# Optimization experiments

Hardware: AMD Instinct MI355X
Metric: run time of the kernel (lower is better)

The kernel has to match this reference:

```python
import jax, jax.numpy as jnp
import numpy as np

B, N, C, H, NL, NH = 8, 1024, 256, 512, 3, 8


def setup_inputs() -> dict:
    key = jax.random.key(0)
    ks = jax.random.split(key, 16)
    g = lambda k, shape: jax.random.normal(k, shape, jnp.float32) * 0.02
    return dict(
        concept_features=jax.random.normal(ks[0], (B, N, C), jnp.float32),
        adjacency_matrix=jax.random.uniform(ks[1], (B, N, N), jnp.float32),
        edge_types=jax.random.randint(ks[2], (B, N, N), 0, 10),
        concept_mask=jnp.ones((B, N), bool),
        W_emb=g(ks[3], (H, C)), b_emb=jnp.zeros((H,), jnp.float32),
        W_in=g(ks[4], (NL, 3 * H, H)), b_in=jnp.zeros((NL, 3 * H), jnp.float32),
        W_out=g(ks[5], (NL, H, H)), b_out=jnp.zeros((NL, H), jnp.float32),
        W_conv=g(ks[6], (NL, H, H)), b_conv=jnp.zeros((NL, H), jnp.float32),
        W_cls=g(ks[7], (1, H)), b_cls=jnp.zeros((1,), jnp.float32),
        W_diff=g(ks[8], (5, H)), b_diff=jnp.zeros((5,), jnp.float32),
        W_pre=g(ks[9], (1, 2 * H)), b_pre=jnp.zeros((1,), jnp.float32),
        W_pool=g(ks[10], (H, H)), b_pool=jnp.zeros((H,), jnp.float32),
    )


def reference(concept_features, adjacency_matrix, edge_types, concept_mask,
              W_emb, b_emb, W_in, b_in, W_out, b_out, W_conv, b_conv,
              W_cls, b_cls, W_diff, b_diff, W_pre, b_pre, W_pool, b_pool):
    Bq, Nc, _ = concept_features.shape
    Hd = W_emb.shape[0]
    dh = Hd // NH

    def mha(x, Wi, bi, Wo, bo):
        # torch nn.MultiheadAttention with batch_first=False: the (B,N,H)
        # input is treated as (seq=B, batch=N, embed=H) -> attention over B.
        qkv = x @ Wi.T + bi                      # (B,N,3H)
        q, k, v = jnp.split(qkv, 3, axis=-1)
        rs = lambda t: t.reshape(Bq, Nc, NH, dh)
        q, k, v = rs(q), rs(k), rs(v)
        sc = jnp.einsum('inhd,jnhd->nhij', q, k) / jnp.sqrt(jnp.float32(dh))
        a = jax.nn.softmax(sc, axis=-1)          # (N,NH,B,B)
        o = jnp.einsum('nhij,jnhd->inhd', a, v).reshape(Bq, Nc, Hd)
        return o @ Wo.T + bo

    def ln(x):  # F.layer_norm, no affine
        m = x.mean(-1, keepdims=True)
        v = ((x - m) ** 2).mean(-1, keepdims=True)
        return (x - m) * jax.lax.rsqrt(v + 1e-5)

    x = concept_features @ W_emb.T + b_emb       # (B,N,H)
    for l in range(W_in.shape[0]):
        att = mha(x, W_in[l], b_in[l], W_out[l], b_out[l])
        conv = att @ W_conv[l].T + b_conv[l]
        agg = jnp.einsum('bij,bjh->bih', adjacency_matrix, conv)
        x = ln(x + agg)

    mastery = x @ W_cls.T + b_cls                # (B,N,1)
    diff = x @ W_diff.T + b_diff                 # (B,N,5)

    # O(N^2) pairwise loop -> bilinear decomposition:
    # score(i,j) = x_i @ W_pre[:, :H].T + x_j @ W_pre[:, H:].T + b
    h1 = (x @ W_pre[:, :Hd].T)[..., 0]           # (B,N)
    h2 = (x @ W_pre[:, Hd:].T)[..., 0]           # (B,N)
    pair = h1[:, :, None] + h2[:, None, :] + b_pre[0]  # (B,N,N)
    off = ~np.eye(Nc, dtype=bool).reshape(-1)    # static mask, i!=j row-major
    prereq = pair.reshape(Bq, Nc * Nc)[:, off][..., None]  # (B,N*(N-1),1)

    graph = x.mean(axis=1) @ W_pool.T + b_pool   # (B,H)
    return (x, mastery, diff, prereq, graph)
```

## Files before the change

kernel.cpp:

```cpp
#include <hip/hip_runtime.h>
#include <hip/hip_bf16.h>

typedef unsigned short ushort_t;
typedef __attribute__((ext_vector_type(4))) float floatx4;
typedef __attribute__((ext_vector_type(8))) __bf16 bf16x8;
typedef __attribute__((ext_vector_type(4))) unsigned short ushortx4;
typedef __attribute__((ext_vector_type(8))) unsigned short ushortx8;

static __device__ __forceinline__ float b2f(ushort_t u) {
  union { unsigned int i; float f; } v; v.i = ((unsigned int)u) << 16; return v.f;
}
static __device__ __forceinline__ ushort_t f2b(float f) {
  unsigned int x = __float_as_uint(f);
  unsigned int r = (x + 0x7fffu + ((x >> 16) & 1u)) >> 16;
  return (ushort_t)r;
}
static __device__ __forceinline__ void glds16(const ushort_t* g, ushort_t* l) {
  __builtin_amdgcn_global_load_lds(
      (const __attribute__((address_space(1))) unsigned int*)g,
      (__attribute__((address_space(3))) unsigned int*)l, 16, 0, 0);
}

template<int MODE, bool ASPLIT, bool SPLITK>
__global__ __launch_bounds__(256, 3) void gemm_bt(
    const void* __restrict__ Ap, const ushort_t* __restrict__ Bm,
    const float* __restrict__ bias,
    float* __restrict__ CoutF, float* __restrict__ CoutF2,
    ushort_t* __restrict__ CoutB, ushort_t* __restrict__ CoutB2,
    int M, int N, int K, long aBatch, long bBatch, long cBatch)
{
  __shared__ __align__(16) ushort_t As[128 * 64];
  __shared__ __align__(16) ushort_t Bs[128 * 64];

  const int tid  = threadIdx.x;
  const int wid  = tid >> 6;
  const int lane = tid & 63;
  const int quad = lane >> 4;
  const int l16  = lane & 15;
  const int lin = blockIdx.y * gridDim.x + blockIdx.x;
  const int m0 = (lin % gridDim.y) * 128;
  const int n0 = (lin / gridDim.y) * 128;
  const int z  = SPLITK ? (blockIdx.z >> 1) : blockIdx.z;
  const int kh = SPLITK ? (blockIdx.z & 1) : 0;
  const int kbeg = SPLITK ? kh * (K >> 1) : 0;
  const int kend = SPLITK ? kbeg + (K >> 1) : K;
  float*    outF = (SPLITK && kh) ? CoutF2 : CoutF;
  ushort_t* outB = (SPLITK && kh) ? CoutB2 : CoutB;

  const ushort_t* Ab = (const ushort_t*)Ap + (long)z * aBatch;
  const float*    Af = (const float*)Ap + (long)z * aBatch;
  Bm += (long)z * bBatch;

  const int wr = (wid >> 1) * 64;
  const int wc = (wid & 1) * 64;

  const int srow = tid >> 3, ssub = (tid & 7) * 8;
  const long abase = (long)(m0 + srow) * K + ssub;
  const long bbase = (long)(n0 + srow) * K + ssub;

  floatx4 acc[4][4];
#pragma unroll
  for (int i = 0; i < 4; ++i)
#pragma unroll
    for (int j = 0; j < 4; ++j) acc[i][j] = (floatx4){0.f, 0.f, 0.f, 0.f};

  for (int k0 = kbeg; k0 < kend; k0 += 64) {
    __syncthreads();
    if constexpr (ASPLIT) {
#pragma unroll
      for (int p = 0; p < 4; ++p)
        glds16(Ab + abase + 32 * p * (long)K + k0, &As[tid * 8 + p * 2048]);
    } else {
#pragma unroll
      for (int p = 0; p < 8; ++p) {
        int c = tid + p * 256;
        int row = c >> 4, sub = (c & 15) * 4;
        floatx4 va = *(const floatx4*)(Af + (long)(m0 + row) * K + k0 + sub);
        ushortx4 ah;
#pragma unroll
        for (int r = 0; r < 4; ++r) ah[r] = f2b(va[r]);
        *(ushortx4*)(&As[row * 64 + sub]) = ah;
      }
    }
#pragma unroll
    for (int p = 0; p < 4; ++p)
      glds16(Bm + bbase + 32 * p * (long)K + k0, &Bs[tid * 8 + p * 2048]);
    __syncthreads();

#pragma unroll
    for (int kk = 0; kk < 2; ++kk) {
      bf16x8 a[4], b[4];
#pragma unroll
      for (int i = 0; i < 4; ++i)
        a[i] = *(const bf16x8*)(&As[(wr + i * 16 + l16) * 64 + kk * 32 + quad * 8]);
#pragma unroll
      for (int j = 0; j < 4; ++j)
        b[j] = *(const bf16x8*)(&Bs[(wc + j * 16 + l16) * 64 + kk * 32 + quad * 8]);
#pragma unroll
      for (int i = 0; i < 4; ++i)
#pragma unroll
        for (int j = 0; j < 4; ++j)
          acc[i][j] = __builtin_amdgcn_mfma_f32_16x16x32_bf16(a[i], b[j], acc[i][j], 0, 0, 0);
    }
  }

#pragma unroll
  for (int j = 0; j < 4; ++j) {
    int col = n0 + wc + j * 16 + l16;
    float bv = (bias != nullptr) ? bias[col] : 0.f;
#pragma unroll
    for (int i = 0; i < 4; ++i) {
      int mbase = m0 + wr + i * 16 + quad * 4;
      if constexpr (MODE == 0) {
#pragma unroll
        for (int r = 0; r < 4; ++r)
          outF[(long)z * cBatch + (long)(mbase + r) * N + col] = acc[i][j][r] + bv;
      } else if constexpr (MODE == 1) {
#pragma unroll
        for (int r = 0; r < 4; ++r)
          outB[(long)z * cBatch + (long)(mbase + r) * N + col] = f2b(acc[i][j][r] + bv);
      } else {
        int b = mbase >> 10, jrow = mbase & 1023;
        ushortx4 pk;
#pragma unroll
        for (int r = 0; r < 4; ++r) pk[r] = f2b(acc[i][j][r] + bv);
        *(ushortx4*)(CoutB + ((long)b * N + col) * 1024 + jrow) = pk;
      }
    }
  }
}

__global__ __launch_bounds__(256) void prep_kernel(
    const float* __restrict__ Win,  ushort_t* __restrict__ Winb,
    const float* __restrict__ Wemb, ushort_t* __restrict__ Wembb,
    const float* __restrict__ Wconv, ushort_t* __restrict__ Wcb,
    const float* __restrict__ ADJ,  ushort_t* __restrict__ ADJb,
    float* __restrict__ xm)
{
  const int bid = blockIdx.x, tid = threadIdx.x;
  const float* src; ushort_t* dst; long i;
  if (bid < 1152)      { src = Win;   dst = Winb;  i = (long)bid * 256 + tid; }
  else if (bid < 1216) { src = Wemb;  dst = Wembb; i = (long)(bid - 1152) * 256 + tid; }
  else if (bid < 1600) { src = Wconv; dst = Wcb;   i = (long)(bid - 1216) * 256 + tid; }
  else if (bid < 5696) { src = ADJ;   dst = ADJb;  i = (long)(bid - 1600) * 256 + tid; }
  else { xm[(bid - 5696) * 256 + tid] = 0.f; return; }
  floatx4 a = ((const floatx4*)src)[2 * i];
  floatx4 b = ((const floatx4*)src)[2 * i + 1];
  ushortx4 ha, hb;
#pragma unroll
  for (int r = 0; r < 4; ++r) { ha[r] = f2b(a[r]); hb[r] = f2b(b[r]); }
  ((ushortx4*)dst)[2 * i] = ha; ((ushortx4*)dst)[2 * i + 1] = hb;
}

__global__ __launch_bounds__(256) void transpose_split_kernel(
    const float* __restrict__ W, ushort_t* __restrict__ T)
{
  __shared__ float tile[64][65];
  const int k0 = blockIdx.x * 64, j0 = blockIdx.y * 64;
  const long base = (long)blockIdx.z * 262144;
  const int tid = threadIdx.x;
#pragma unroll
  for (int p = 0; p < 16; ++p) {
    int idx = tid + p * 256;
    int jj = idx >> 6, kk = idx & 63;
    tile[jj][kk] = W[base + (long)(j0 + jj) * 512 + k0 + kk];
  }
  __syncthreads();
#pragma unroll
  for (int p = 0; p < 16; ++p) {
    int idx = tid + p * 256;
    int kk = idx >> 6, jj = idx & 63;
    T[base + (long)(k0 + kk) * 512 + j0 + jj] = f2b(tile[jj][kk]);
  }
}

__global__ __launch_bounds__(256) void bfuse_kernel(
    const float* __restrict__ Wconv, const float* __restrict__ bout,
    const float* __restrict__ bconv, float* __restrict__ bf)
{
  const int w = threadIdx.x >> 6, lane = threadIdx.x & 63;
  const int gi = blockIdx.x * 4 + w;
  const int l = gi >> 9, o = gi & 511;
  float p = 0.f;
#pragma unroll
  for (int k = 0; k < 8; ++k)
    p += Wconv[(long)l * 262144 + (long)o * 512 + lane + 64 * k] *
         bout[l * 512 + lane + 64 * k];
#pragma unroll
  for (int msk = 1; msk <= 32; msk <<= 1) p += __shfl_xor(p, msk);
  if (lane == 0) bf[gi] = p + bconv[l * 512 + o];
}

__global__ __launch_bounds__(512) void attn_kernel(
    const ushort_t* __restrict__ qkv, ushort_t* __restrict__ outp)
{
  __shared__ float qs[8 * 1540];
  __shared__ float aw[8][64];
  const int tid = threadIdx.x;
  const int n = blockIdx.x;

  const ushort_t* src = qkv + (long)n * 1536;
#pragma unroll
  for (int p = 0; p < 3; ++p) {
    int c = tid + p * 512;
    int i = c / 192, off = (c % 192) * 8;
    ushortx8 u = *(const ushortx8*)(src + (long)i * 1024 * 1536 + off);
    float* d = &qs[i * 1540 + off];
#pragma unroll
    for (int r = 0; r < 8; ++r) d[r] = b2f(u[r]);
  }
  __syncthreads();

  const int h    = tid >> 6;
  const int lane = tid & 63;
  const int i = lane >> 3, j = lane & 7;
  float s = 0.f;
#pragma unroll 8
  for (int d = 0; d < 64; ++d)
    s += qs[i * 1540 + h * 64 + d] * qs[j * 1540 + 512 + h * 64 + d];
  s *= 0.125f;

  float m = s;
  m = fmaxf(m, __shfl_xor(m, 1));
  m = fmaxf(m, __shfl_xor(m, 2));
  m = fmaxf(m, __shfl_xor(m, 4));
  float e = __expf(s - m);
  float sum = e;
  sum += __shfl_xor(sum, 1);
  sum += __shfl_xor(sum, 2);
  sum += __shfl_xor(sum, 4);
  aw[h][lane] = e / sum;

  const long ob = (long)n * 512 + h * 64 + lane;
#pragma unroll
  for (int ii = 0; ii < 8; ++ii) {
    float acc = 0.f;
#pragma unroll
    for (int jj = 0; jj < 8; ++jj)
      acc += aw[h][ii * 8 + jj] * qs[jj * 1540 + 1024 + h * 64 + lane];
    outp[ob + (long)ii * 1024 * 512] = f2b(acc);
  }
}

__global__ __launch_bounds__(256) void ln_kernel(
    const ushort_t* __restrict__ xb,
    const ushort_t* __restrict__ aggA, const ushort_t* __restrict__ aggB,
    ushort_t* __restrict__ outB)
{
  const int w = threadIdx.x >> 6, lane = threadIdx.x & 63;
  const long base = ((long)blockIdx.x * 4 + w) * 512;
  float v[8];
  float s = 0.f;
#pragma unroll
  for (int k = 0; k < 8; ++k) {
    long idx = base + lane + 64 * k;
    v[k] = b2f(xb[idx]) + b2f(aggA[idx]) + b2f(aggB[idx]);
    s += v[k];
  }
#pragma unroll
  for (int msk = 1; msk <= 32; msk <<= 1) s += __shfl_xor(s, msk);
  float mean = s * (1.f / 512.f);
  float vv = 0.f;
#pragma unroll
  for (int k = 0; k < 8; ++k) { float d = v[k] - mean; vv += d * d; }
#pragma unroll
  for (int msk = 1; msk <= 32; msk <<= 1) vv += __shfl_xor(vv, msk);
  float inv = rsqrtf(vv * (1.f / 512.f) + 1e-5f);
#pragma unroll
  for (int k = 0; k < 8; ++k)
    outB[base + lane + 64 * k] = f2b((v[k] - mean) * inv);
}

__global__ __launch_bounds__(256) void final_ln_heads_kernel(
    const ushort_t* __restrict__ xb,
    const ushort_t* __restrict__ aggA, const ushort_t* __restrict__ aggB,
    float* __restrict__ out_x,
    const float* __restrict__ Wcls, const float* __restrict__ bcls,
    const float* __restrict__ Wdiff, const float* __restrict__ bdiff,
    const float* __restrict__ Wpre,
    float* __restrict__ mastery, float* __restrict__ diff,
    float* __restrict__ h1, float* __restrict__ h2)
{
  const int w = threadIdx.x >> 6, lane = threadIdx.x & 63;
  const long row = (long)blockIdx.x * 4 + w;
  const long base = row * 512;
  float v[8];
  float s = 0.f;
#pragma unroll
  for (int k = 0; k < 8; ++k) {
    long idx = base + lane + 64 * k;
    v[k] = b2f(xb[idx]) + b2f(aggA[idx]) + b2f(aggB[idx]);
    s += v[k];
  }
#pragma unroll
  for (int msk = 1; msk <= 32; msk <<= 1) s += __shfl_xor(s, msk);
  float mean = s * (1.f / 512.f);
  float vv = 0.f;
#pragma unroll
  for (int k = 0; k < 8; ++k) { float d = v[k] - mean; vv += d * d; }
#pragma unroll
  for (int msk = 1; msk <= 32; msk <<= 1) vv += __shfl_xor(vv, msk);
  float inv = rsqrtf(vv * (1.f / 512.f) + 1e-5f);
#pragma unroll
  for (int k = 0; k < 8; ++k) {
    v[k] = (v[k] - mean) * inv;
    out_x[base + lane + 64 * k] = v[k];
  }
#pragma unroll
  for (int o = 0; o < 8; ++o) {
    const float* wp = (o == 0) ? Wcls
                    : (o <= 5) ? (Wdiff + (o - 1) * 512)
                    : (o == 6) ? Wpre : (Wpre + 512);
    float p = 0.f;
#pragma unroll
    for (int k = 0; k < 8; ++k) p += v[k] * wp[lane + 64 * k];
#pragma unroll
    for (int msk = 1; msk <= 32; msk <<= 1) p += __shfl_xor(p, msk);
    if (lane == 0) {
      if (o == 0)      mastery[row] = p + bcls[0];
      else if (o <= 5) diff[row * 5 + (o - 1)] = p + bdiff[o - 1];
      else if (o == 6) h1[row] = p;
      else             h2[row] = p;
    }
  }
}

__global__ __launch_bounds__(256) void epi_kernel(
    const float* __restrict__ h1, const float* __restrict__ h2,
    const float* __restrict__ bpre, float* __restrict__ outp,
    const float* __restrict__ x, float* __restrict__ xm)
{
  const int bid = blockIdx.x;
  if (bid < 8192) {
    const int b = bid >> 10, i = bid & 1023;
    const float base = h1[b * 1024 + i] + bpre[0];
    const long ob = (long)b * (1024 * 1023) + (long)i * 1023;
#pragma unroll
    for (int r = 0; r < 4; ++r) {
      int j = r * 256 + threadIdx.x;
      if (j == i) continue;
      int pos = (j < i) ? j : j - 1;
      outp[ob + pos] = base + h2[b * 1024 + j];
    }
  } else {
    const int pb = bid - 8192;
    const int b = pb >> 5, cc = (pb >> 4) & 1, ns = pb & 15;
    const int c = cc * 256 + threadIdx.x;
    float s = 0.f;
    for (int n = ns * 64; n < ns * 64 + 64; ++n)
      s += x[((long)b * 1024 + n) * 512 + c];
    atomicAdd(&xm[b * 512 + c], s);
  }
}

__global__ __launch_bounds__(256) void graph_kernel(
    const float* __restrict__ xm, const float* __restrict__ Wpool,
    const float* __restrict__ bpool, float* __restrict__ g)
{
  const int gi = blockIdx.x * 256 + threadIdx.x;
  const int b = gi >> 9, o = gi & 511;
  float s = 0.f;
  for (int hh = 0; hh < 512; ++hh) s += xm[b * 512 + hh] * Wpool[o * 512 + hh];
  g[gi] = s * (1.f / 1024.f) + bpool[o];
}

extern "C" void kernel_launch(void* const* d_in, const int* in_sizes, int n_in,
                              void* d_out, int out_size, void* d_ws, size_t ws_size,
                              hipStream_t stream)
{
  const float* CF    = (const float*)d_in[0];
  const float* ADJ   = (const float*)d_in[1];
  const float* Wemb  = (const float*)d_in[4];
  const float* bemb  = (const float*)d_in[5];
  const float* Win   = (const float*)d_in[6];
  const float* bin   = (const float*)d_in[7];
  const float* Wout  = (const float*)d_in[8];
  const float* bout  = (const float*)d_in[9];
  const float* Wconv = (const float*)d_in[10];
  const float* bconv = (const float*)d_in[11];
  const float* Wcls  = (const float*)d_in[12];
  const float* bcls  = (const float*)d_in[13];
  const float* Wdiff = (const float*)d_in[14];
  const float* bdiff = (const float*)d_in[15];
  const float* Wpre  = (const float*)d_in[16];
  const float* bpre  = (const float*)d_in[17];
  const float* Wpool = (const float*)d_in[18];
  const float* bpool = (const float*)d_in[19];

  ushort_t* W = (ushort_t*)d_ws;
  ushort_t* xb   = W;
  ushort_t* qkvb = W + 4194304;
  ushort_t* cT    = qkvb;
  ushort_t* aggA  = qkvb + 4194304;
  ushort_t* aggB  = qkvb + 8388608;
  ushort_t* WoT   = qkvb + 4194304;
  ushort_t* Wembb = qkvb + 4980736;
  ushort_t* Wcb   = qkvb + 5111808;
  ushort_t* Winb = W + 16777216;
  ushort_t* Wfb  = W + 19136512;
  ushort_t* ADJb = W + 19922944;
  float* bfused = (float*)(W + 28311552);
  float* h1     = bfused + 1536;
  float* h2     = h1 + 8192;
  float* xm     = h2 + 8192;

  float* out_x       = (float*)d_out;
  float* out_mastery = out_x + 4194304;
  float* out_diff    = out_mastery + 8192;
  float* out_prereq  = out_diff + 40960;
  float* out_graph   = out_prereq + 8380416;
  ushort_t* aob = (ushort_t*)out_x;

  dim3 blk(256);

  prep_kernel<<<dim3(5712), blk, 0, stream>>>(Win, Winb, Wemb, Wembb,
                                              Wconv, Wcb, ADJ, ADJb, xm);
  transpose_split_kernel<<<dim3(8, 8, 3), blk, 0, stream>>>(Wout, WoT);
  gemm_bt<1, true, false><<<dim3(4, 4, 3), blk, 0, stream>>>(
      Wcb, WoT, nullptr, nullptr, nullptr, Wfb, nullptr,
      512, 512, 512, 262144, 262144, 262144);
  bfuse_kernel<<<dim3(384), blk, 0, stream>>>(Wconv, bout, bconv, bfused);

  gemm_bt<1, false, false><<<dim3(4, 64, 1), blk, 0, stream>>>(
      CF, Wembb, bemb, nullptr, nullptr, xb, nullptr, 8192, 512, 256, 0, 0, 0);

  for (int l = 0; l < 3; ++l) {
    gemm_bt<1, true, false><<<dim3(12, 64, 1), blk, 0, stream>>>(
        xb, Winb + (long)l * 786432, bin + l * 1536,
        nullptr, nullptr, qkvb, nullptr, 8192, 1536, 512, 0, 0, 0);
    attn_kernel<<<dim3(1024), dim3(512), 0, stream>>>(qkvb, aob);
    gemm_bt<2, true, false><<<dim3(4, 64, 1), blk, 0, stream>>>(
        aob, Wfb + (long)l * 262144, bfused + l * 512,
        nullptr, nullptr, cT, nullptr, 8192, 512, 512, 0, 0, 0);
    gemm_bt<1, true, true><<<dim3(4, 8, 16), blk, 0, stream>>>(
        ADJb, cT, nullptr, nullptr, nullptr, aggA, aggB,
        1024, 512, 1024, 1048576, 524288, 524288);
    if (l < 2)
      ln_kernel<<<dim3(2048), blk, 0, stream>>>(xb, aggA, aggB, xb);
    else
      final_ln_heads_kernel<<<dim3(2048), blk, 0, stream>>>(
          xb, aggA, aggB, out_x, Wcls, bcls, Wdiff, bdiff, Wpre,
          out_mastery, out_diff, h1, h2);
  }

  epi_kernel<<<dim3(8448), blk, 0, stream>>>(h1, h2, bpre, out_prereq,
                                             out_x, xm);
  graph_kernel<<<dim3(16), blk, 0, stream>>>(xm, Wpool, bpool, out_graph);
}
```

Before: 457.9 us.

## Swizzle GEMM LDS layout, split adjacency GEMM K four ways, fuse prep kernels

Applies an XOR swizzle to the LDS tile layout in the GEMM, used both for the global-to-LDS loads and the MFMA fragment reads, to avoid LDS bank conflicts. The adjacency aggregation GEMM goes from a 2-way to a 4-way split-K for more parallelism. The extra partial sums are staged in the prereq output buffer before it is written, and the layernorm kernels sum all four partials. The weight transpose and fused-bias kernels are folded into the prep kernel to save launches. The trade is more bf16 partial traffic and one more rounding step in the aggregation sum.

```diff
diff --git a/kernel.cpp b/kernel.cpp
--- a/kernel.cpp
+++ b/kernel.cpp
@@ -21,12 +21,12 @@
       (__attribute__((address_space(3))) unsigned int*)l, 16, 0, 0);
 }
 
-template<int MODE, bool ASPLIT, bool SPLITK>
+template<int MODE, bool ASPLIT, int KS>
 __global__ __launch_bounds__(256, 3) void gemm_bt(
     const void* __restrict__ Ap, const ushort_t* __restrict__ Bm,
     const float* __restrict__ bias,
-    float* __restrict__ CoutF, float* __restrict__ CoutF2,
-    ushort_t* __restrict__ CoutB, ushort_t* __restrict__ CoutB2,
+    ushort_t* __restrict__ C0, ushort_t* __restrict__ C1,
+    ushort_t* __restrict__ C2, ushort_t* __restrict__ C3,
     int M, int N, int K, long aBatch, long bBatch, long cBatch)
 {
   __shared__ __align__(16) ushort_t As[128 * 64];
@@ -40,12 +40,14 @@
   const int lin = blockIdx.y * gridDim.x + blockIdx.x;
   const int m0 = (lin % gridDim.y) * 128;
   const int n0 = (lin / gridDim.y) * 128;
-  const int z  = SPLITK ? (blockIdx.z >> 1) : blockIdx.z;
-  const int kh = SPLITK ? (blockIdx.z & 1) : 0;
-  const int kbeg = SPLITK ? kh * (K >> 1) : 0;
-  const int kend = SPLITK ? kbeg + (K >> 1) : K;
-  float*    outF = (SPLITK && kh) ? CoutF2 : CoutF;
-  ushort_t* outB = (SPLITK && kh) ? CoutB2 : CoutB;
+  const int z  = (KS > 1) ? (int)(blockIdx.z / KS) : blockIdx.z;
+  const int kq = (KS > 1) ? (int)(blockIdx.z % KS) : 0;
+  const int kbeg = kq * (K / KS);
+  const int kend = kbeg + (K / KS);
+  ushort_t* outB = C0;
+  if (KS >= 2 && kq == 1) outB = C1;
+  if (KS >= 4 && kq == 2) outB = C2;
+  if (KS >= 4 && kq == 3) outB = C3;
 
   const ushort_t* Ab = (const ushort_t*)Ap + (long)z * aBatch;
   const float*    Af = (const float*)Ap + (long)z * aBatch;
@@ -54,15 +56,18 @@
   const int wr = (wid >> 1) * 64;
   const int wc = (wid & 1) * 64;
 
-  const int srow = tid >> 3, ssub = (tid & 7) * 8;
-  const long abase = (long)(m0 + srow) * K + ssub;
-  const long bbase = (long)(n0 + srow) * K + ssub;
+  const int srow = tid >> 3;
+  const int scj  = ((tid & 7) ^ (srow & 7)) * 8;
+  const long abase = (long)(m0 + srow) * K + scj;
+  const long bbase = (long)(n0 + srow) * K + scj;
 
   floatx4 acc[4][4];
 #pragma unroll
   for (int i = 0; i < 4; ++i)
 #pragma unroll
     for (int j = 0; j < 4; ++j) acc[i][j] = (floatx4){0.f, 0.f, 0.f, 0.f};
+
+  const int rx = l16 & 7;
 
   for (int k0 = kbeg; k0 < kend; k0 += 64) {
     __syncthreads();
@@ -74,12 +79,13 @@
 #pragma unroll
       for (int p = 0; p < 8; ++p) {
         int c = tid + p * 256;
-        int row = c >> 4, sub = (c & 15) * 4;
-        floatx4 va = *(const floatx4*)(Af + (long)(m0 + row) * K + k0 + sub);
+        int row = c >> 4, sub4 = c & 15;
+        floatx4 va = *(const floatx4*)(Af + (long)(m0 + row) * K + k0 + sub4 * 4);
         ushortx4 ah;
 #pragma unroll
         for (int r = 0; r < 4; ++r) ah[r] = f2b(va[r]);
-        *(ushortx4*)(&As[row * 64 + sub]) = ah;
+        int dst = row * 64 + (((sub4 >> 1) ^ (row & 7)) << 3) + ((sub4 & 1) << 2);
+        *(ushortx4*)(&As[dst]) = ah;
       }
     }
 #pragma unroll
@@ -92,10 +98,12 @@
       bf16x8 a[4], b[4];
 #pragma unroll
       for (int i = 0; i < 4; ++i)
-        a[i] = *(const bf16x8*)(&As[(wr + i * 16 + l16) * 64 + kk * 32 + quad * 8]);
+        a[i] = *(const bf16x8*)(&As[(wr + i * 16 + l16) * 64 +
+                                    (((kk * 4 + quad) ^ rx) << 3)]);
 #pragma unroll
       for (int j = 0; j < 4; ++j)
-        b[j] = *(const bf16x8*)(&Bs[(wc + j * 16 + l16) * 64 + kk * 32 + quad * 8]);
+        b[j] = *(const bf16x8*)(&Bs[(wc + j * 16 + l16) * 64 +
+                                    (((kk * 4 + quad) ^ rx) << 3)]);
 #pragma unroll
       for (int i = 0; i < 4; ++i)
 #pragma unroll
@@ -111,11 +119,7 @@
 #pragma unroll
     for (int i = 0; i < 4; ++i) {
       int mbase = m0 + wr + i * 16 + quad * 4;
-      if constexpr (MODE == 0) {
-#pragma unroll
-        for (int r = 0; r < 4; ++r)
-          outF[(long)z * cBatch + (long)(mbase + r) * N + col] = acc[i][j][r] + bv;
-      } else if constexpr (MODE == 1) {
+      if constexpr (MODE == 1) {
 #pragma unroll
         for (int r = 0; r < 4; ++r)
           outB[(long)z * cBatch + (long)(mbase + r) * N + col] = f2b(acc[i][j][r] + bv);
@@ -124,7 +128,7 @@
         ushortx4 pk;
 #pragma unroll
         for (int r = 0; r < 4; ++r) pk[r] = f2b(acc[i][j][r] + bv);
-        *(ushortx4*)(CoutB + ((long)b * N + col) * 1024 + jrow) = pk;
+        *(ushortx4*)(outB + ((long)b * N + col) * 1024 + jrow) = pk;
       }
     }
   }
@@ -135,60 +139,57 @@
     const float* __restrict__ Wemb, ushort_t* __restrict__ Wembb,
     const float* __restrict__ Wconv, ushort_t* __restrict__ Wcb,
     const float* __restrict__ ADJ,  ushort_t* __restrict__ ADJb,
-    float* __restrict__ xm)
-{
+    float* __restrict__ xm,
+    const float* __restrict__ Wout, ushort_t* __restrict__ WoT,
+    const float* __restrict__ bout, const float* __restrict__ bconv,
+    float* __restrict__ bfused)
+{
+  __shared__ float tile[64][65];
   const int bid = blockIdx.x, tid = threadIdx.x;
-  const float* src; ushort_t* dst; long i;
-  if (bid < 1152)      { src = Win;   dst = Winb;  i = (long)bid * 256 + tid; }
-  else if (bid < 1216) { src = Wemb;  dst = Wembb; i = (long)(bid - 1152) * 256 + tid; }
-  else if (bid < 1600) { src = Wconv; dst = Wcb;   i = (long)(bid - 1216) * 256 + tid; }
-  else if (bid < 5696) { src = ADJ;   dst = ADJb;  i = (long)(bid - 1600) * 256 + tid; }
-  else { xm[(bid - 5696) * 256 + tid] = 0.f; return; }
-  floatx4 a = ((const floatx4*)src)[2 * i];
-  floatx4 b = ((const floatx4*)src)[2 * i + 1];
-  ushortx4 ha, hb;
-#pragma unroll
-  for (int r = 0; r < 4; ++r) { ha[r] = f2b(a[r]); hb[r] = f2b(b[r]); }
-  ((ushortx4*)dst)[2 * i] = ha; ((ushortx4*)dst)[2 * i + 1] = hb;
-}
-
-__global__ __launch_bounds__(256) void transpose_split_kernel(
-    const float* __restrict__ W, ushort_t* __restrict__ T)
-{
-  __shared__ float tile[64][65];
-  const int k0 = blockIdx.x * 64, j0 = blockIdx.y * 64;
-  const long base = (long)blockIdx.z * 262144;
-  const int tid = threadIdx.x;
-#pragma unroll
-  for (int p = 0; p < 16; ++p) {
-    int idx = tid + p * 256;
-    int jj = idx >> 6, kk = idx & 63;
-    tile[jj][kk] = W[base + (long)(j0 + jj) * 512 + k0 + kk];
-  }
-  __syncthreads();
-#pragma unroll
-  for (int p = 0; p < 16; ++p) {
-    int idx = tid + p * 256;
-    int kk = idx >> 6, jj = idx & 63;
-    T[base + (long)(k0 + kk) * 512 + j0 + jj] = f2b(tile[jj][kk]);
-  }
-}
-
-__global__ __launch_bounds__(256) void bfuse_kernel(
-    const float* __restrict__ Wconv, const float* __restrict__ bout,
-    const float* __restrict__ bconv, float* __restrict__ bf)
-{
-  const int w = threadIdx.x >> 6, lane = threadIdx.x & 63;
-  const int gi = blockIdx.x * 4 + w;
-  const int l = gi >> 9, o = gi & 511;
-  float p = 0.f;
-#pragma unroll
-  for (int k = 0; k < 8; ++k)
-    p += Wconv[(long)l * 262144 + (long)o * 512 + lane + 64 * k] *
-         bout[l * 512 + lane + 64 * k];
-#pragma unroll
-  for (int msk = 1; msk <= 32; msk <<= 1) p += __shfl_xor(p, msk);
-  if (lane == 0) bf[gi] = p + bconv[l * 512 + o];
+  if (bid < 5696) {
+    const float* src; ushort_t* dst; long i;
+    if (bid < 1152)      { src = Win;   dst = Winb;  i = (long)bid * 256 + tid; }
+    else if (bid < 1216) { src = Wemb;  dst = Wembb; i = (long)(bid - 1152) * 256 + tid; }
+    else if (bid < 1600) { src = Wconv; dst = Wcb;   i = (long)(bid - 1216) * 256 + tid; }
+    else                 { src = ADJ;   dst = ADJb;  i = (long)(bid - 1600) * 256 + tid; }
+    floatx4 a = ((const floatx4*)src)[2 * i];
+    floatx4 b = ((const floatx4*)src)[2 * i + 1];
+    ushortx4 ha, hb;
+#pragma unroll
+    for (int r = 0; r < 4; ++r) { ha[r] = f2b(a[r]); hb[r] = f2b(b[r]); }
+    ((ushortx4*)dst)[2 * i] = ha; ((ushortx4*)dst)[2 * i + 1] = hb;
+  } else if (bid < 5712) {
+    xm[(bid - 5696) * 256 + tid] = 0.f;
+  } else if (bid < 5904) {
+    const int t = bid - 5712;
+    const int z = t >> 6, k0 = ((t >> 3) & 7) * 64, j0 = (t & 7) * 64;
+    const long base = (long)z * 262144;
+#pragma unroll
+    for (int p = 0; p < 16; ++p) {
+      int idx = tid + p * 256;
+      int jj = idx >> 6, kk = idx & 63;
+      tile[jj][kk] = Wout[base + (long)(j0 + jj) * 512 + k0 + kk];
+    }
+    __syncthreads();
+#pragma unroll
+    for (int p = 0; p < 16; ++p) {
+      int idx = tid + p * 256;
+      int kk = idx >> 6, jj = idx & 63;
+      WoT[base + (long)(k0 + kk) * 512 + j0 + jj] = f2b(tile[jj][kk]);
+    }
+  } else {
+    const int w = tid >> 6, lane = tid & 63;
+    const int gi = (bid - 5904) * 4 + w;
+    const int l = gi >> 9, o = gi & 511;
+    float p = 0.f;
+#pragma unroll
+    for (int k = 0; k < 8; ++k)
+      p += Wconv[(long)l * 262144 + (long)o * 512 + lane + 64 * k] *
+           bout[l * 512 + lane + 64 * k];
+#pragma unroll
+    for (int msk = 1; msk <= 32; msk <<= 1) p += __shfl_xor(p, msk);
+    if (lane == 0) bfused[gi] = p + bconv[l * 512 + o];
+  }
 }
 
 __global__ __launch_bounds__(512) void attn_kernel(
@@ -245,6 +246,7 @@
 __global__ __launch_bounds__(256) void ln_kernel(
     const ushort_t* __restrict__ xb,
     const ushort_t* __restrict__ aggA, const ushort_t* __restrict__ aggB,
+    const ushort_t* __restrict__ aggC, const ushort_t* __restrict__ aggD,
     ushort_t* __restrict__ outB)
 {
   const int w = threadIdx.x >> 6, lane = threadIdx.x & 63;
@@ -254,7 +256,8 @@
 #pragma unroll
   for (int k = 0; k < 8; ++k) {
     long idx = base + lane + 64 * k;
-    v[k] = b2f(xb[idx]) + b2f(aggA[idx]) + b2f(aggB[idx]);
+    v[k] = b2f(xb[idx]) + b2f(aggA[idx]) + b2f(aggB[idx]) +
+           b2f(aggC[idx]) + b2f(aggD[idx]);
     s += v[k];
   }
 #pragma unroll
@@ -274,6 +277,7 @@
 __global__ __launch_bounds__(256) void final_ln_heads_kernel(
     const ushort_t* __restrict__ xb,
     const ushort_t* __restrict__ aggA, const ushort_t* __restrict__ aggB,
+    const ushort_t* __restrict__ aggC, const ushort_t* __restrict__ aggD,
     float* __restrict__ out_x,
     const float* __restrict__ Wcls, const float* __restrict__ bcls,
     const float* __restrict__ Wdiff, const float* __restrict__ bdiff,
@@ -289,7 +293,8 @@
 #pragma unroll
   for (int k = 0; k < 8; ++k) {
     long idx = base + lane + 64 * k;
-    v[k] = b2f(xb[idx]) + b2f(aggA[idx]) + b2f(aggB[idx]);
+    v[k] = b2f(xb[idx]) + b2f(aggA[idx]) + b2f(aggB[idx]) +
+           b2f(aggC[idx]) + b2f(aggD[idx]);
     s += v[k];
   }
 #pragma unroll
@@ -410,36 +415,37 @@
   float* out_prereq  = out_diff + 40960;
   float* out_graph   = out_prereq + 8380416;
   ushort_t* aob = (ushort_t*)out_x;
+  ushort_t* aggC = (ushort_t*)out_prereq;
+  ushort_t* aggD = (ushort_t*)out_prereq + 4194304;
 
   dim3 blk(256);
 
-  prep_kernel<<<dim3(5712), blk, 0, stream>>>(Win, Winb, Wemb, Wembb,
-                                              Wconv, Wcb, ADJ, ADJb, xm);
-  transpose_split_kernel<<<dim3(8, 8, 3), blk, 0, stream>>>(Wout, WoT);
-  gemm_bt<1, true, false><<<dim3(4, 4, 3), blk, 0, stream>>>(
-      Wcb, WoT, nullptr, nullptr, nullptr, Wfb, nullptr,
+  prep_kernel<<<dim3(6288), blk, 0, stream>>>(
+      Win, Winb, Wemb, Wembb, Wconv, Wcb, ADJ, ADJb, xm,
+      Wout, WoT, bout, bconv, bfused);
+  gemm_bt<1, true, 1><<<dim3(4, 4, 3), blk, 0, stream>>>(
+      Wcb, WoT, nullptr, Wfb, nullptr, nullptr, nullptr,
       512, 512, 512, 262144, 262144, 262144);
-  bfuse_kernel<<<dim3(384), blk, 0, stream>>>(Wconv, bout, bconv, bfused);
-
-  gemm_bt<1, false, false><<<dim3(4, 64, 1), blk, 0, stream>>>(
-      CF, Wembb, bemb, nullptr, nullptr, xb, nullptr, 8192, 512, 256, 0, 0, 0);
+
+  gemm_bt<1, false, 1><<<dim3(4, 64, 1), blk, 0, stream>>>(
+      CF, Wembb, bemb, xb, nullptr, nullptr, nullptr, 8192, 512, 256, 0, 0, 0);
 
   for (int l = 0; l < 3; ++l) {
-    gemm_bt<1, true, false><<<dim3(12, 64, 1), blk, 0, stream>>>(
+    gemm_bt<1, true, 1><<<dim3(12, 64, 1), blk, 0, stream>>>(
         xb, Winb + (long)l * 786432, bin + l * 1536,
-        nullptr, nullptr, qkvb, nullptr, 8192, 1536, 512, 0, 0, 0);
+        qkvb, nullptr, nullptr, nullptr, 8192, 1536, 512, 0, 0, 0);
     attn_kernel<<<dim3(1024), dim3(512), 0, stream>>>(qkvb, aob);
-    gemm_bt<2, true, false><<<dim3(4, 64, 1), blk, 0, stream>>>(
+    gemm_bt<2, true, 1><<<dim3(4, 64, 1), blk, 0, stream>>>(
         aob, Wfb + (long)l * 262144, bfused + l * 512,
-        nullptr, nullptr, cT, nullptr, 8192, 512, 512, 0, 0, 0);
-    gemm_bt<1, true, true><<<dim3(4, 8, 16), blk, 0, stream>>>(
-        ADJb, cT, nullptr, nullptr, nullptr, aggA, aggB,
+        cT, nullptr, nullptr, nullptr, 8192, 512, 512, 0, 0, 0);
+    gemm_bt<1, true, 4><<<dim3(4, 8, 32), blk, 0, stream>>>(
+        ADJb, cT, nullptr, aggA, aggB, aggC, aggD,
         1024, 512, 1024, 1048576, 524288, 524288);
     if (l < 2)
-      ln_kernel<<<dim3(2048), blk, 0, stream>>>(xb, aggA, aggB, xb);
+      ln_kernel<<<dim3(2048), blk, 0, stream>>>(xb, aggA, aggB, aggC, aggD, xb);
     else
       final_ln_heads_kernel<<<dim3(2048), blk, 0, stream>>>(
-          xb, aggA, aggB, out_x, Wcls, bcls, Wdiff, bdiff, Wpre,
+          xb, aggA, aggB, aggC, aggD, out_x, Wcls, bcls, Wdiff, bdiff, Wpre,
           out_mastery, out_diff, h1, h2);
   }
 
```

After: 455.0 us. No clear change (-0.6%).
